# Kernel tuning notes

Hardware: AMD Instinct MI355X
Metric: run time of the kernel (lower is better)

## Reference

```python
import jax, jax.numpy as jnp
import numpy as np

HID = 1280
CROSS = 2048
HEAD_DIM = 64
N_HEADS = HID // HEAD_DIM  # 20
FF = 4 * HID               # 5120
EPS = 1e-5


def _layernorm(x, g, b):
    mu = jnp.mean(x, axis=-1, keepdims=True)
    var = jnp.mean(jnp.square(x - mu), axis=-1, keepdims=True)
    return (x - mu) * jax.lax.rsqrt(var + EPS) * g + b


def _attention(x_q, x_kv, wq, wk, wv, wo, bo):
    b, t, _ = x_q.shape
    q = x_q @ wq.T  # [b,t,HID]
    k = x_kv @ wk.T
    v = x_kv @ wv.T
    q = q.reshape(b, t, N_HEADS, HEAD_DIM).transpose(0, 2, 1, 3)
    s = x_kv.shape[1]
    k = k.reshape(b, s, N_HEADS, HEAD_DIM).transpose(0, 2, 1, 3)
    v = v.reshape(b, s, N_HEADS, HEAD_DIM).transpose(0, 2, 1, 3)
    scale = HEAD_DIM ** -0.5
    scores = jnp.einsum('bhtd,bhsd->bhts', q, k) * scale
    attn = jax.nn.softmax(scores, axis=-1)
    o = jnp.einsum('bhts,bhsd->bhtd', attn, v)
    o = o.transpose(0, 2, 1, 3).reshape(b, t, HID)
    return o @ wo.T + bo


def setup_inputs() -> dict:
    key = jax.random.key(0)
    ks = jax.random.split(key, 16)
    std = 0.02
    d = {}
    d['x'] = jax.random.normal(ks[0], (2, 2048, HID), jnp.float32)
    d['encoder_hidden_states'] = jax.random.normal(ks[1], (2, 77, CROSS), jnp.float32)
    d['ln1_g'] = jnp.ones((HID,), jnp.float32); d['ln1_b'] = jnp.zeros((HID,), jnp.float32)
    d['ln2_g'] = jnp.ones((HID,), jnp.float32); d['ln2_b'] = jnp.zeros((HID,), jnp.float32)
    d['ln3_g'] = jnp.ones((HID,), jnp.float32); d['ln3_b'] = jnp.zeros((HID,), jnp.float32)
    d['wq1'] = jax.random.normal(ks[2], (HID, HID), jnp.float32) * std
    d['wk1'] = jax.random.normal(ks[3], (HID, HID), jnp.float32) * std
    d['wv1'] = jax.random.normal(ks[4], (HID, HID), jnp.float32) * std
    d['wo1'] = jax.random.normal(ks[5], (HID, HID), jnp.float32) * std
    d['bo1'] = jnp.zeros((HID,), jnp.float32)
    d['wq2'] = jax.random.normal(ks[6], (HID, HID), jnp.float32) * std
    d['wk2'] = jax.random.normal(ks[7], (HID, CROSS), jnp.float32) * std
    d['wv2'] = jax.random.normal(ks[8], (HID, CROSS), jnp.float32) * std
    d['wo2'] = jax.random.normal(ks[9], (HID, HID), jnp.float32) * std
    d['bo2'] = jnp.zeros((HID,), jnp.float32)
    d['w_geglu'] = jax.random.normal(ks[10], (2 * FF, HID), jnp.float32) * std
    d['b_geglu'] = jnp.zeros((2 * FF,), jnp.float32)
    d['w_ffout'] = jax.random.normal(ks[11], (HID, FF), jnp.float32) * std
    d['b_ffout'] = jnp.zeros((HID,), jnp.float32)
    return d


def reference(x, encoder_hidden_states,
              ln1_g, ln1_b, ln2_g, ln2_b, ln3_g, ln3_b,
              wq1, wk1, wv1, wo1, bo1,
              wq2, wk2, wv2, wo2, bo2,
              w_geglu, b_geglu, w_ffout, b_ffout):
    # self-attention
    h = _layernorm(x, ln1_g, ln1_b)
    x = x + _attention(h, h, wq1, wk1, wv1, wo1, bo1)
    # cross-attention
    h = _layernorm(x, ln2_g, ln2_b)
    x = x + _attention(h, encoder_hidden_states, wq2, wk2, wv2, wo2, bo2)
    # GEGLU feed-forward
    h = _layernorm(x, ln3_g, ln3_b)
    proj = h @ w_geglu.T + b_geglu  # [b,t,2*FF]
    x1, x2 = proj[..., :FF], proj[..., FF:]
    ff = (x1 * jax.nn.gelu(x2, approximate=False)) @ w_ffout.T + b_ffout
    return x + ff
```

## Files before the change

### kernel.cpp

```cpp
#include <hip/hip_runtime.h>

typedef unsigned short u16;
typedef __bf16 bf16x8 __attribute__((ext_vector_type(8)));
typedef float f32x4 __attribute__((ext_vector_type(4)));

#define HID 1280
#define NHEADS 20
#define FFD 5120

__device__ __forceinline__ u16 f2b(float f) {
  union { float f; unsigned u; } a; a.f = f;
  unsigned r = a.u + 0x7FFFu + ((a.u >> 16) & 1u);
  return (u16)(r >> 16);
}

__device__ __forceinline__ void g2lds16(const void* g, void* l) {
  __builtin_amdgcn_global_load_lds(
      (__attribute__((address_space(1))) void*)(g),
      (__attribute__((address_space(3))) void*)(l), 16, 0, 0);
}

__device__ __forceinline__ void swz(int& bx, int& by) {
  int nx = gridDim.x, ny = gridDim.y;
  int id = blockIdx.y * nx + blockIdx.x;
  int sx = ((nx & 7) == 0) ? 8 : (((nx & 3) == 0) ? 4 : (((nx & 1) == 0) ? 2 : 1));
  int sy = ((ny & 7) == 0) ? 8 : (((ny & 3) == 0) ? 4 : (((ny & 1) == 0) ? 2 : 1));
  int per = sx * sy;
  int st = id / per, w = id - st * per;
  int nsx = nx / sx;
  int stx = st % nsx, sty = st / nsx;
  bx = stx * sx + (w % sx);
  by = sty * sy + (w / sx);
}

struct CvtArgs {
  const float* src[10];
  u16* dst[10];
  int cum4[11];
};

__global__ __launch_bounds__(256) void cvt_weights(CvtArgs a, int total4) {
  int i = blockIdx.x * 256 + threadIdx.x;
  if (i >= total4) return;
  int seg = 0;
#pragma unroll
  for (int s = 1; s < 10; s++) seg += (i >= a.cum4[s]);
  int j = (i - a.cum4[seg]) * 4;
  float4 f = *(const float4*)(a.src[seg] + j);
  union { unsigned long long u; u16 s[4]; } o;
  o.s[0] = f2b(f.x); o.s[1] = f2b(f.y); o.s[2] = f2b(f.z); o.s[3] = f2b(f.w);
  *(unsigned long long*)(a.dst[seg] + j) = o.u;
}

__global__ __launch_bounds__(256) void cvt_enc(const float* __restrict__ enc,
                                               u16* __restrict__ encp) {
  int i = blockIdx.x * 256 + threadIdx.x;
  int j = i * 4;
  int row = j >> 11;
  unsigned long long out = 0ull;
  if (row < 154) {
    float4 f = *(const float4*)(enc + j);
    union { unsigned long long u; u16 s[4]; } o;
    o.s[0] = f2b(f.x); o.s[1] = f2b(f.y); o.s[2] = f2b(f.z); o.s[3] = f2b(f.w);
    out = o.u;
  }
  *(unsigned long long*)(encp + j) = out;
}

__global__ __launch_bounds__(256) void ln_bf16(const float* __restrict__ X,
                                               const float* __restrict__ g,
                                               const float* __restrict__ bta,
                                               u16* __restrict__ Out) {
  const int row = blockIdx.x, tid = threadIdx.x;
  const float* xr = X + (size_t)row * HID;
  float v[5];
#pragma unroll
  for (int i = 0; i < 5; i++) v[i] = xr[tid + i * 256];
  float s = v[0] + v[1] + v[2] + v[3] + v[4];
#pragma unroll
  for (int off = 32; off >= 1; off >>= 1) s += __shfl_down(s, off);
  __shared__ float red[4];
  if ((tid & 63) == 0) red[tid >> 6] = s;
  __syncthreads();
  float mu = (red[0] + red[1] + red[2] + red[3]) * (1.0f / HID);
  float d = 0.f;
#pragma unroll
  for (int i = 0; i < 5; i++) { float t = v[i] - mu; d += t * t; }
#pragma unroll
  for (int off = 32; off >= 1; off >>= 1) d += __shfl_down(d, off);
  __syncthreads();
  if ((tid & 63) == 0) red[tid >> 6] = d;
  __syncthreads();
  float rstd = rsqrtf((red[0] + red[1] + red[2] + red[3]) * (1.0f / HID) + 1e-5f);
#pragma unroll
  for (int i = 0; i < 5; i++) {
    int c = tid + i * 256;
    Out[(size_t)row * HID + c] = f2b((v[i] - mu) * rstd * g[c] + bta[c]);
  }
}

__global__ __launch_bounds__(256) void gemm_bt(
    const u16* __restrict__ A, const u16* __restrict__ Bw,
    u16* __restrict__ Cb, float* __restrict__ Cf,
    const float* __restrict__ bias, const float* __restrict__ resid,
    int M, int N, int K, int mode, int nsplit) {
  __shared__ u16 As[4096];
  __shared__ u16 Bs[4096];
  const int tid = threadIdx.x;
  const int wid = tid >> 6, lane = tid & 63;
  const int quad = lane >> 4, l16 = lane & 15;
  int bx, by; swz(bx, by);
  const int bm = by * 128, bn = bx * 128;
  const int wm = (wid & 1) * 64, wn = (wid >> 1) * 64;

  const int arow = tid >> 2;
  const int acol = (((tid & 3) ^ ((tid >> 2) & 3)) * 8);
  const u16* Ag0 = A + (size_t)(bm + arow) * K + acol;
  const u16* Ag1 = A + (size_t)(bm + 64 + arow) * K + acol;
  const u16* Bg0 = Bw + (size_t)(bn + arow) * K + acol;
  const u16* Bg1 = Bw + (size_t)(bn + 64 + arow) * K + acol;
  u16* ldsA0 = &As[wid * 512];
  u16* ldsA1 = &As[2048 + wid * 512];
  u16* ldsB0 = &Bs[wid * 512];
  u16* ldsB1 = &Bs[2048 + wid * 512];

  f32x4 acc[4][4] = {};
  const int fsw = (quad ^ (l16 & 3)) * 8;

  for (int k0 = 0; k0 < K; k0 += 32) {
    __syncthreads();
    g2lds16(Ag0 + k0, ldsA0);
    g2lds16(Ag1 + k0, ldsA1);
    g2lds16(Bg0 + k0, ldsB0);
    g2lds16(Bg1 + k0, ldsB1);
    __syncthreads();
    bf16x8 af[4], bfr[4];
#pragma unroll
    for (int mt = 0; mt < 4; mt++)
      af[mt] = *(const bf16x8*)&As[(wm + mt * 16 + l16) * 32 + fsw];
#pragma unroll
    for (int nt = 0; nt < 4; nt++)
      bfr[nt] = *(const bf16x8*)&Bs[(wn + nt * 16 + l16) * 32 + fsw];
#pragma unroll
    for (int mt = 0; mt < 4; mt++)
#pragma unroll
      for (int nt = 0; nt < 4; nt++)
        acc[mt][nt] = __builtin_amdgcn_mfma_f32_16x16x32_bf16(af[mt], bfr[nt], acc[mt][nt], 0, 0, 0);
  }

  if (mode == 0) {
#pragma unroll
    for (int mt = 0; mt < 4; mt++)
#pragma unroll
      for (int nt = 0; nt < 4; nt++)
#pragma unroll
        for (int r = 0; r < 4; r++) {
          int row = bm + wm + mt * 16 + quad * 4 + r;
          int col = bn + wn + nt * 16 + l16;
          u16 val = f2b(acc[mt][nt][r]);
          if (nsplit > 0) {
            int t = (col >= 2 * nsplit) ? 2 : ((col >= nsplit) ? 1 : 0);
            int dc = col - t * nsplit;
            Cb[(size_t)t * M * nsplit + (size_t)row * nsplit + dc] = val;
          } else {
            Cb[(size_t)row * N + col] = val;
          }
        }
  } else {
#pragma unroll
    for (int mt = 0; mt < 4; mt++)
#pragma unroll
      for (int nt = 0; nt < 4; nt++)
#pragma unroll
        for (int r = 0; r < 4; r++) {
          int row = bm + wm + mt * 16 + quad * 4 + r;
          int col = bn + wn + nt * 16 + l16;
          size_t idx = (size_t)row * N + col;
          Cf[idx] = acc[mt][nt][r] + bias[col] + resid[idx];
        }
  }
}

__global__ __launch_bounds__(256) void gemm_geglu(
    const u16* __restrict__ A, const u16* __restrict__ W,
    const float* __restrict__ bias, u16* __restrict__ Out,
    int M, int K) {
  __shared__ u16 As[4096];
  __shared__ u16 B1s[2048];
  __shared__ u16 B2s[2048];
  const int tid = threadIdx.x;
  const int wid = tid >> 6, lane = tid & 63;
  const int quad = lane >> 4, l16 = lane & 15;
  int bx, by; swz(bx, by);
  const int bm = by * 128, bn = bx * 64;
  const int wm = (wid & 1) * 64, wn = (wid >> 1) * 32;

  const int arow = tid >> 2;
  const int acol = (((tid & 3) ^ ((tid >> 2) & 3)) * 8);
  const u16* Ag0 = A + (size_t)(bm + arow) * K + acol;
  const u16* Ag1 = A + (size_t)(bm + 64 + arow) * K + acol;
  const u16* B1g = W + (size_t)(bn + arow) * K + acol;
  const u16* B2g = W + (size_t)(FFD + bn + arow) * K + acol;

  f32x4 acc1[4][2] = {};
  f32x4 acc2[4][2] = {};
  const int fsw = (quad ^ (l16 & 3)) * 8;

  for (int k0 = 0; k0 < K; k0 += 32) {
    __syncthreads();
    g2lds16(Ag0 + k0, &As[wid * 512]);
    g2lds16(Ag1 + k0, &As[2048 + wid * 512]);
    g2lds16(B1g + k0, &B1s[wid * 512]);
    g2lds16(B2g + k0, &B2s[wid * 512]);
    __syncthreads();
    bf16x8 af[4], b1[2], b2[2];
#pragma unroll
    for (int mt = 0; mt < 4; mt++)
      af[mt] = *(const bf16x8*)&As[(wm + mt * 16 + l16) * 32 + fsw];
#pragma unroll
    for (int nt = 0; nt < 2; nt++) {
      b1[nt] = *(const bf16x8*)&B1s[(wn + nt * 16 + l16) * 32 + fsw];
      b2[nt] = *(const bf16x8*)&B2s[(wn + nt * 16 + l16) * 32 + fsw];
    }
#pragma unroll
    for (int mt = 0; mt < 4; mt++)
#pragma unroll
      for (int nt = 0; nt < 2; nt++) {
        acc1[mt][nt] = __builtin_amdgcn_mfma_f32_16x16x32_bf16(af[mt], b1[nt], acc1[mt][nt], 0, 0, 0);
        acc2[mt][nt] = __builtin_amdgcn_mfma_f32_16x16x32_bf16(af[mt], b2[nt], acc2[mt][nt], 0, 0, 0);
      }
  }

#pragma unroll
  for (int mt = 0; mt < 4; mt++)
#pragma unroll
    for (int nt = 0; nt < 2; nt++)
#pragma unroll
      for (int r = 0; r < 4; r++) {
        int row = bm + wm + mt * 16 + quad * 4 + r;
        int col = bn + wn + nt * 16 + l16;
        float v1 = acc1[mt][nt][r] + bias[col];
        float v2 = acc2[mt][nt][r] + bias[FFD + col];
        float ge = 0.5f * v2 * (1.0f + erff(v2 * 0.70710678118654752440f));
        Out[(size_t)row * FFD + col] = f2b(v1 * ge);
      }
}

#define BS 128
__global__ __launch_bounds__(256) void flash_attn(
    const u16* __restrict__ Q, const u16* __restrict__ Kb,
    const u16* __restrict__ Vb, u16* __restrict__ O,
    int T, int Sv, float scale) {
  __shared__ u16 Ks[BS * 64];
  __shared__ u16 Vt[64 * BS];
  __shared__ u16 Ps[4][16 * BS];
  const int tid = threadIdx.x, wid = tid >> 6, lane = tid & 63;
  const int quad = lane >> 4, l16 = lane & 15;
  const int b = blockIdx.y / NHEADS, h = blockIdx.y % NHEADS;
  const int q0 = blockIdx.x * 64;

  const size_t qrow = (size_t)(b * T + q0 + wid * 16 + l16);
  bf16x8 aq0 = *(const bf16x8*)&Q[qrow * HID + h * 64 + quad * 8];
  bf16x8 aq1 = *(const bf16x8*)&Q[qrow * HID + h * 64 + 32 + quad * 8];
#pragma unroll
  for (int j = 0; j < 8; j++) {
    aq0[j] = (__bf16)((float)aq0[j] * scale);
    aq1[j] = (__bf16)((float)aq1[j] * scale);
  }
  bf16x8 ones;
#pragma unroll
  for (int j = 0; j < 8; j++) ones[j] = (__bf16)1.0f;

  f32x4 oacc[4] = {};
  float m_i[4], l_i[4];
#pragma unroll
  for (int r = 0; r < 4; r++) { m_i[r] = -1.0e30f; l_i[r] = 0.f; }

  const int ntiles = (Sv + BS - 1) / BS;
  for (int t0 = 0; t0 < ntiles; ++t0) {
    const int srow0 = b * Sv + t0 * BS;
    __syncthreads();
#pragma unroll
    for (int c = 0; c < 4; ++c) {
      int slot = c * 256 + tid;
      int row = slot >> 3, p = slot & 7;
      int gsrc = p ^ (row & 7);
      g2lds16(Kb + (size_t)(srow0 + row) * HID + h * 64 + gsrc * 8,
              &Ks[(size_t)(c * 256 + wid * 64) * 8]);
    }
#pragma unroll
    for (int c = 0; c < 4; ++c) {
      int slot = c * 256 + tid;
      int srow = slot >> 3, scol = (slot & 7) * 8;
      union { uint4 u; u16 e[8]; } vv;
      vv.u = *(const uint4*)&Vb[(size_t)(srow0 + srow) * HID + h * 64 + scol];
      int g = srow >> 3, so = srow & 7;
#pragma unroll
      for (int j = 0; j < 8; j++) {
        int d = scol + j;
        int f = ((d >> 3) ^ d) & 7;
        Vt[d * BS + ((g ^ f) * 8 + so)] = vv.e[j];
      }
    }
    __syncthreads();

    f32x4 sc[8];
#pragma unroll
    for (int nt = 0; nt < 8; nt++) {
      int s = nt * 16 + l16;
      int fb = (s & 7) ;
      bf16x8 bk0 = *(const bf16x8*)&Ks[s * 64 + ((quad ^ fb) * 8)];
      bf16x8 bk1 = *(const bf16x8*)&Ks[s * 64 + (((quad ^ 4) ^ fb) * 8)];
      f32x4 z = {0.f, 0.f, 0.f, 0.f};
      z = __builtin_amdgcn_mfma_f32_16x16x32_bf16(aq0, bk0, z, 0, 0, 0);
      z = __builtin_amdgcn_mfma_f32_16x16x32_bf16(aq1, bk1, z, 0, 0, 0);
      sc[nt] = z;
    }
    if ((t0 == ntiles - 1) && (Sv & (BS - 1))) {
#pragma unroll
      for (int nt = 0; nt < 8; nt++) {
        int s = t0 * BS + nt * 16 + l16;
        if (s >= Sv)
#pragma unroll
          for (int r = 0; r < 4; r++) sc[nt][r] = -1.0e30f;
      }
    }
    float mnew[4];
#pragma unroll
    for (int r = 0; r < 4; r++) mnew[r] = m_i[r];
#pragma unroll
    for (int nt = 0; nt < 8; nt++)
#pragma unroll
      for (int r = 0; r < 4; r++) mnew[r] = fmaxf(mnew[r], sc[nt][r]);
#pragma unroll
    for (int off = 8; off >= 1; off >>= 1)
#pragma unroll
      for (int r = 0; r < 4; r++) mnew[r] = fmaxf(mnew[r], __shfl_xor(mnew[r], off));

    float alpha[4];
#pragma unroll
    for (int r = 0; r < 4; r++) alpha[r] = __expf(m_i[r] - mnew[r]);
#pragma unroll
    for (int nt = 0; nt < 8; nt++)
#pragma unroll
      for (int r = 0; r < 4; r++) sc[nt][r] = __expf(sc[nt][r] - mnew[r]);

#pragma unroll
    for (int nt = 0; nt < 8; nt++)
#pragma unroll
      for (int r = 0; r < 4; r++) {
        int row = quad * 4 + r, col = nt * 16 + l16;
        int g = col >> 3;
        Ps[wid][row * BS + ((g ^ (row & 7)) * 8 + (col & 7))] = f2b(sc[nt][r]);
      }
    bf16x8 pa[4];
#pragma unroll
    for (int kc = 0; kc < 4; kc++) {
      int lg = kc * 4 + quad;
      pa[kc] = *(const bf16x8*)&Ps[wid][l16 * BS + ((lg ^ (l16 & 7)) * 8)];
    }
    f32x4 ls = {0.f, 0.f, 0.f, 0.f};
#pragma unroll
    for (int kc = 0; kc < 4; kc++)
      ls = __builtin_amdgcn_mfma_f32_16x16x32_bf16(pa[kc], ones, ls, 0, 0, 0);
#pragma unroll
    for (int r = 0; r < 4; r++) {
      l_i[r] = l_i[r] * alpha[r] + ls[r];
      m_i[r] = mnew[r];
    }
#pragma unroll
    for (int dt = 0; dt < 4; dt++)
#pragma unroll
      for (int r = 0; r < 4; r++) oacc[dt][r] *= alpha[r];

#pragma unroll
    for (int dt = 0; dt < 4; dt++) {
      int d = dt * 16 + l16;
      int f = ((d >> 3) ^ d) & 7;
#pragma unroll
      for (int kc = 0; kc < 4; kc++) {
        int lg = kc * 4 + quad;
        bf16x8 bv = *(const bf16x8*)&Vt[d * BS + ((lg ^ f) * 8)];
        oacc[dt] = __builtin_amdgcn_mfma_f32_16x16x32_bf16(pa[kc], bv, oacc[dt], 0, 0, 0);
      }
    }
  }

#pragma unroll
  for (int dt = 0; dt < 4; dt++)
#pragma unroll
    for (int r = 0; r < 4; r++) {
      int row = b * T + q0 + wid * 16 + quad * 4 + r;
      int col = h * 64 + dt * 16 + l16;
      O[(size_t)row * HID + col] = f2b(oacc[dt][r] / l_i[r]);
    }
}

extern "C" void kernel_launch(void* const* d_in, const int* in_sizes, int n_in,
                              void* d_out, int out_size, void* d_ws, size_t ws_size,
                              hipStream_t stream) {
  const float* x    = (const float*)d_in[0];
  const float* enc  = (const float*)d_in[1];
  const float* ln1g = (const float*)d_in[2];
  const float* ln1b = (const float*)d_in[3];
  const float* ln2g = (const float*)d_in[4];
  const float* ln2b = (const float*)d_in[5];
  const float* ln3g = (const float*)d_in[6];
  const float* ln3b = (const float*)d_in[7];
  const float* wq1  = (const float*)d_in[8];
  const float* wk1  = (const float*)d_in[9];
  const float* wv1  = (const float*)d_in[10];
  const float* wo1  = (const float*)d_in[11];
  const float* bo1  = (const float*)d_in[12];
  const float* wq2  = (const float*)d_in[13];
  const float* wk2  = (const float*)d_in[14];
  const float* wv2  = (const float*)d_in[15];
  const float* wo2  = (const float*)d_in[16];
  const float* bo2  = (const float*)d_in[17];
  const float* wg   = (const float*)d_in[18];
  const float* bg   = (const float*)d_in[19];
  const float* wf   = (const float*)d_in[20];
  const float* bfo  = (const float*)d_in[21];
  float* out = (float*)d_out;

  const size_t S1 = 1280 * 1280;
  const size_t S2 = 1280 * 2048;
  const size_t SG = 10240 * 1280;
  const size_t SF = 1280 * 5120;
  const size_t ACT = (size_t)4096 * 1280;

  char* ws = (char*)d_ws;
  size_t off = 0;
  auto alloc = [&](size_t bytes) -> void* {
    void* p = ws + off;
    off += (bytes + 255) & ~(size_t)255;
    return p;
  };
  u16* wq1b = (u16*)alloc(S1 * 2);
  u16* wk1b = (u16*)alloc(S1 * 2);
  u16* wv1b = (u16*)alloc(S1 * 2);
  u16* wo1b = (u16*)alloc(S1 * 2);
  u16* wq2b = (u16*)alloc(S1 * 2);
  u16* wk2b = (u16*)alloc(S2 * 2);
  u16* wv2b = (u16*)alloc(S2 * 2);
  u16* wo2b = (u16*)alloc(S1 * 2);
  u16* wgb  = (u16*)alloc(SG * 2);
  u16* wfb  = (u16*)alloc(SF * 2);
  u16* h    = (u16*)alloc(ACT * 2);
  u16* q    = (u16*)alloc(ACT * 2);
  u16* k    = (u16*)alloc(ACT * 2);
  u16* v    = (u16*)alloc(ACT * 2);
  u16* o    = (u16*)alloc(ACT * 2);
  u16* ffin = q;
  u16* k2   = (u16*)alloc((size_t)256 * 1280 * 2);
  u16* v2   = (u16*)alloc((size_t)256 * 1280 * 2);
  u16* encp = (u16*)alloc((size_t)256 * 2048 * 2);
  float* x2 = out;
  float* x3 = (float*)alloc(ACT * 4);
  (void)k; (void)v; (void)ws_size; (void)in_sizes; (void)n_in; (void)out_size;

  CvtArgs ca;
  const float* srcs[10] = {wq1, wk1, wv1, wo1, wq2, wk2, wv2, wo2, wg, wf};
  u16* dsts[10] = {wq1b, wk1b, wv1b, wo1b, wq2b, wk2b, wv2b, wo2b, wgb, wfb};
  int n4s[10] = {(int)(S1/4), (int)(S1/4), (int)(S1/4), (int)(S1/4), (int)(S1/4),
                 (int)(S2/4), (int)(S2/4), (int)(S1/4), (int)(SG/4), (int)(SF/4)};
  ca.cum4[0] = 0;
  for (int i = 0; i < 10; i++) { ca.src[i] = srcs[i]; ca.dst[i] = dsts[i]; ca.cum4[i+1] = ca.cum4[i] + n4s[i]; }
  int total4 = ca.cum4[10];
  cvt_weights<<<(total4 + 255) / 256, 256, 0, stream>>>(ca, total4);
  cvt_enc<<<512, 256, 0, stream>>>(enc, encp);

  ln_bf16<<<4096, 256, 0, stream>>>(x, ln1g, ln1b, h);
  gemm_bt<<<dim3(30, 32), 256, 0, stream>>>(h, wq1b, q, nullptr, nullptr, nullptr,
                                            4096, 3840, 1280, 0, 1280);
  flash_attn<<<dim3(32, 40), 256, 0, stream>>>(q, k, v, o, 2048, 2048, 0.125f);
  gemm_bt<<<dim3(10, 32), 256, 0, stream>>>(o, wo1b, nullptr, x2, bo1, x,
                                            4096, 1280, 1280, 1, 0);
  ln_bf16<<<4096, 256, 0, stream>>>(x2, ln2g, ln2b, h);
  gemm_bt<<<dim3(10, 32), 256, 0, stream>>>(h, wq2b, q, nullptr, nullptr, nullptr,
                                            4096, 1280, 1280, 0, 0);
  gemm_bt<<<dim3(20, 2), 256, 0, stream>>>(encp, wk2b, k2, nullptr, nullptr, nullptr,
                                           256, 2560, 2048, 0, 1280);
  flash_attn<<<dim3(32, 40), 256, 0, stream>>>(q, k2, v2, o, 2048, 77, 0.125f);
  gemm_bt<<<dim3(10, 32), 256, 0, stream>>>(o, wo2b, nullptr, x3, bo2, x2,
                                            4096, 1280, 1280, 1, 0);
  ln_bf16<<<4096, 256, 0, stream>>>(x3, ln3g, ln3b, h);
  gemm_geglu<<<dim3(80, 32), 256, 0, stream>>>(h, wgb, bg, ffin, 4096, 1280);
  gemm_bt<<<dim3(10, 32), 256, 0, stream>>>(ffin, wfb, nullptr, out, bfo, x3,
                                            4096, 1280, 5120, 1, 0);
}
```

Before: 884.3 us.

## Double GEMM K-tile to 64 with new swizzle and use fast GELU

Both GEMM kernels now stage 64-wide K slices into LDS per iteration instead of 32. They use a new 8-way XOR swizzle and two MFMA sub-steps per slice, halving the barrier and loop overhead per unit of work while doubling LDS use. The GEGLU epilogue swaps erf-based GELU for a tanh-style sigmoid approximation, which is cheaper but deviates slightly from the exact reference.

```diff
diff --git a/kernel.cpp b/kernel.cpp
--- a/kernel.cpp
+++ b/kernel.cpp
@@ -12,6 +12,11 @@
   union { float f; unsigned u; } a; a.f = f;
   unsigned r = a.u + 0x7FFFu + ((a.u >> 16) & 1u);
   return (u16)(r >> 16);
+}
+
+__device__ __forceinline__ float gelu_fast(float x) {
+  float z = 1.5957691216f * (x + 0.044715f * x * x * x);
+  return x / (1.0f + __expf(-z));
 }
 
 __device__ __forceinline__ void g2lds16(const void* g, void* l) {
@@ -104,8 +109,8 @@
     u16* __restrict__ Cb, float* __restrict__ Cf,
     const float* __restrict__ bias, const float* __restrict__ resid,
     int M, int N, int K, int mode, int nsplit) {
-  __shared__ u16 As[4096];
-  __shared__ u16 Bs[4096];
+  __shared__ u16 As[8192];
+  __shared__ u16 Bs[8192];
   const int tid = threadIdx.x;
   const int wid = tid >> 6, lane = tid & 63;
   const int quad = lane >> 4, l16 = lane & 15;
@@ -113,39 +118,43 @@
   const int bm = by * 128, bn = bx * 128;
   const int wm = (wid & 1) * 64, wn = (wid >> 1) * 64;
 
-  const int arow = tid >> 2;
-  const int acol = (((tid & 3) ^ ((tid >> 2) & 3)) * 8);
-  const u16* Ag0 = A + (size_t)(bm + arow) * K + acol;
-  const u16* Ag1 = A + (size_t)(bm + 64 + arow) * K + acol;
-  const u16* Bg0 = Bw + (size_t)(bn + arow) * K + acol;
-  const u16* Bg1 = Bw + (size_t)(bn + 64 + arow) * K + acol;
-  u16* ldsA0 = &As[wid * 512];
-  u16* ldsA1 = &As[2048 + wid * 512];
-  u16* ldsB0 = &Bs[wid * 512];
-  u16* ldsB1 = &Bs[2048 + wid * 512];
+  size_t aoff[4], boff[4];
+#pragma unroll
+  for (int c = 0; c < 4; ++c) {
+    int g = c * 256 + tid;
+    int row = g >> 3, pg = g & 7;
+    int sc = (pg ^ (row & 7)) * 8;
+    aoff[c] = (size_t)(bm + row) * K + sc;
+    boff[c] = (size_t)(bn + row) * K + sc;
+  }
 
   f32x4 acc[4][4] = {};
-  const int fsw = (quad ^ (l16 & 3)) * 8;
-
-  for (int k0 = 0; k0 < K; k0 += 32) {
+  const int s7 = l16 & 7;
+
+  for (int k0 = 0; k0 < K; k0 += 64) {
     __syncthreads();
-    g2lds16(Ag0 + k0, ldsA0);
-    g2lds16(Ag1 + k0, ldsA1);
-    g2lds16(Bg0 + k0, ldsB0);
-    g2lds16(Bg1 + k0, ldsB1);
+#pragma unroll
+    for (int c = 0; c < 4; ++c) {
+      g2lds16(A + aoff[c] + k0, &As[(c * 256 + wid * 64) * 8]);
+      g2lds16(Bw + boff[c] + k0, &Bs[(c * 256 + wid * 64) * 8]);
+    }
     __syncthreads();
-    bf16x8 af[4], bfr[4];
-#pragma unroll
-    for (int mt = 0; mt < 4; mt++)
-      af[mt] = *(const bf16x8*)&As[(wm + mt * 16 + l16) * 32 + fsw];
-#pragma unroll
-    for (int nt = 0; nt < 4; nt++)
-      bfr[nt] = *(const bf16x8*)&Bs[(wn + nt * 16 + l16) * 32 + fsw];
-#pragma unroll
-    for (int mt = 0; mt < 4; mt++)
+#pragma unroll
+    for (int kc = 0; kc < 2; kc++) {
+      const int ph = ((kc << 2) + quad) ^ s7;
+      bf16x8 af[4], bfr[4];
+#pragma unroll
+      for (int mt = 0; mt < 4; mt++)
+        af[mt] = *(const bf16x8*)&As[(wm + mt * 16 + l16) * 64 + ph * 8];
 #pragma unroll
       for (int nt = 0; nt < 4; nt++)
-        acc[mt][nt] = __builtin_amdgcn_mfma_f32_16x16x32_bf16(af[mt], bfr[nt], acc[mt][nt], 0, 0, 0);
+        bfr[nt] = *(const bf16x8*)&Bs[(wn + nt * 16 + l16) * 64 + ph * 8];
+#pragma unroll
+      for (int mt = 0; mt < 4; mt++)
+#pragma unroll
+        for (int nt = 0; nt < 4; nt++)
+          acc[mt][nt] = __builtin_amdgcn_mfma_f32_16x16x32_bf16(af[mt], bfr[nt], acc[mt][nt], 0, 0, 0);
+    }
   }
 
   if (mode == 0) {
@@ -185,9 +194,9 @@
     const u16* __restrict__ A, const u16* __restrict__ W,
     const float* __restrict__ bias, u16* __restrict__ Out,
     int M, int K) {
-  __shared__ u16 As[4096];
-  __shared__ u16 B1s[2048];
-  __shared__ u16 B2s[2048];
+  __shared__ u16 As[8192];
+  __shared__ u16 B1s[4096];
+  __shared__ u16 B2s[4096];
   const int tid = threadIdx.x;
   const int wid = tid >> 6, lane = tid & 63;
   const int quad = lane >> 4, l16 = lane & 15;
@@ -195,40 +204,54 @@
   const int bm = by * 128, bn = bx * 64;
   const int wm = (wid & 1) * 64, wn = (wid >> 1) * 32;
 
-  const int arow = tid >> 2;
-  const int acol = (((tid & 3) ^ ((tid >> 2) & 3)) * 8);
-  const u16* Ag0 = A + (size_t)(bm + arow) * K + acol;
-  const u16* Ag1 = A + (size_t)(bm + 64 + arow) * K + acol;
-  const u16* B1g = W + (size_t)(bn + arow) * K + acol;
-  const u16* B2g = W + (size_t)(FFD + bn + arow) * K + acol;
+  size_t aoff[4], b1off[2], b2off[2];
+#pragma unroll
+  for (int c = 0; c < 4; ++c) {
+    int g = c * 256 + tid;
+    int row = g >> 3, pg = g & 7;
+    int sc = (pg ^ (row & 7)) * 8;
+    aoff[c] = (size_t)(bm + row) * K + sc;
+    if (c < 2) {
+      b1off[c] = (size_t)(bn + row) * K + sc;
+      b2off[c] = (size_t)(FFD + bn + row) * K + sc;
+    }
+  }
 
   f32x4 acc1[4][2] = {};
   f32x4 acc2[4][2] = {};
-  const int fsw = (quad ^ (l16 & 3)) * 8;
-
-  for (int k0 = 0; k0 < K; k0 += 32) {
+  const int s7 = l16 & 7;
+
+  for (int k0 = 0; k0 < K; k0 += 64) {
     __syncthreads();
-    g2lds16(Ag0 + k0, &As[wid * 512]);
-    g2lds16(Ag1 + k0, &As[2048 + wid * 512]);
-    g2lds16(B1g + k0, &B1s[wid * 512]);
-    g2lds16(B2g + k0, &B2s[wid * 512]);
+#pragma unroll
+    for (int c = 0; c < 4; ++c)
+      g2lds16(A + aoff[c] + k0, &As[(c * 256 + wid * 64) * 8]);
+#pragma unroll
+    for (int c = 0; c < 2; ++c) {
+      g2lds16(W + b1off[c] + k0, &B1s[(c * 256 + wid * 64) * 8]);
+      g2lds16(W + b2off[c] + k0, &B2s[(c * 256 + wid * 64) * 8]);
+    }
     __syncthreads();
-    bf16x8 af[4], b1[2], b2[2];
-#pragma unroll
-    for (int mt = 0; mt < 4; mt++)
-      af[mt] = *(const bf16x8*)&As[(wm + mt * 16 + l16) * 32 + fsw];
-#pragma unroll
-    for (int nt = 0; nt < 2; nt++) {
-      b1[nt] = *(const bf16x8*)&B1s[(wn + nt * 16 + l16) * 32 + fsw];
-      b2[nt] = *(const bf16x8*)&B2s[(wn + nt * 16 + l16) * 32 + fsw];
-    }
-#pragma unroll
-    for (int mt = 0; mt < 4; mt++)
+#pragma unroll
+    for (int kc = 0; kc < 2; kc++) {
+      const int ph = ((kc << 2) + quad) ^ s7;
+      bf16x8 af[4], b1[2], b2[2];
+#pragma unroll
+      for (int mt = 0; mt < 4; mt++)
+        af[mt] = *(const bf16x8*)&As[(wm + mt * 16 + l16) * 64 + ph * 8];
 #pragma unroll
       for (int nt = 0; nt < 2; nt++) {
-        acc1[mt][nt] = __builtin_amdgcn_mfma_f32_16x16x32_bf16(af[mt], b1[nt], acc1[mt][nt], 0, 0, 0);
-        acc2[mt][nt] = __builtin_amdgcn_mfma_f32_16x16x32_bf16(af[mt], b2[nt], acc2[mt][nt], 0, 0, 0);
+        b1[nt] = *(const bf16x8*)&B1s[(wn + nt * 16 + l16) * 64 + ph * 8];
+        b2[nt] = *(const bf16x8*)&B2s[(wn + nt * 16 + l16) * 64 + ph * 8];
       }
+#pragma unroll
+      for (int mt = 0; mt < 4; mt++)
+#pragma unroll
+        for (int nt = 0; nt < 2; nt++) {
+          acc1[mt][nt] = __builtin_amdgcn_mfma_f32_16x16x32_bf16(af[mt], b1[nt], acc1[mt][nt], 0, 0, 0);
+          acc2[mt][nt] = __builtin_amdgcn_mfma_f32_16x16x32_bf16(af[mt], b2[nt], acc2[mt][nt], 0, 0, 0);
+        }
+    }
   }
 
 #pragma unroll
@@ -241,8 +264,7 @@
         int col = bn + wn + nt * 16 + l16;
         float v1 = acc1[mt][nt][r] + bias[col];
         float v2 = acc2[mt][nt][r] + bias[FFD + col];
-        float ge = 0.5f * v2 * (1.0f + erff(v2 * 0.70710678118654752440f));
-        Out[(size_t)row * FFD + col] = f2b(v1 * ge);
+        Out[(size_t)row * FFD + col] = f2b(v1 * gelu_fast(v2));
       }
 }
 
@@ -308,7 +330,7 @@
 #pragma unroll
     for (int nt = 0; nt < 8; nt++) {
       int s = nt * 16 + l16;
-      int fb = (s & 7) ;
+      int fb = (s & 7);
       bf16x8 bk0 = *(const bf16x8*)&Ks[s * 64 + ((quad ^ fb) * 8)];
       bf16x8 bk1 = *(const bf16x8*)&Ks[s * 64 + (((quad ^ 4) ^ fb) * 8)];
       f32x4 z = {0.f, 0.f, 0.f, 0.f};
```

Measured after the change: 807.1 us. 1.1x faster.
